# Optimization experiments

Hardware: AMD Instinct MI355X
Metric: run time of the kernel (lower is better)

## Reference

```python
import jax, jax.numpy as jnp
import numpy as np

N_NODES = 100000
N_EDGES = 1600000
D_IN = 128
D_HID = 128
N_CLASSES = 40


def _glorot(key, fan_in, fan_out):
    lim = np.sqrt(6.0 / (fan_in + fan_out)).astype(np.float32)
    return jax.random.uniform(key, (fan_in, fan_out), jnp.float32, -lim, lim)


def setup_inputs() -> dict:
    key = jax.random.key(0)
    ks = jax.random.split(key, 10)
    x = jax.random.normal(ks[0], (N_NODES, D_IN), jnp.float32)
    edge_index = jax.random.randint(ks[1], (2, N_EDGES), 0, N_NODES, jnp.int64)
    return {
        "x": x,
        "edge_index": edge_index,
        # layer 1: lin_l (neighbor, with bias), lin_r (root, no bias)
        "W1l": _glorot(ks[2], D_IN, D_HID),
        "b1": jnp.zeros((D_HID,), jnp.float32),
        "W1r": _glorot(ks[3], D_IN, D_HID),
        # layer 2
        "W2l": _glorot(ks[4], D_HID, D_HID),
        "b2": jnp.zeros((D_HID,), jnp.float32),
        "W2r": _glorot(ks[5], D_HID, D_HID),
        # layer 3
        "W3l": _glorot(ks[6], D_HID, N_CLASSES),
        "b3": jnp.zeros((N_CLASSES,), jnp.float32),
        "W3r": _glorot(ks[7], D_HID, N_CLASSES),
    }


def _sage_conv(x, src, dst, deg_inv, Wl, bl, Wr):
    # mean aggregation of source-node features onto destination nodes
    msgs = x[src]                                            # [E, d] gather
    agg = jax.ops.segment_sum(msgs, dst, num_segments=N_NODES)  # [N, d]
    agg = agg * deg_inv[:, None]                             # mean
    return agg @ Wl + bl + x @ Wr


def reference(x, edge_index, W1l, b1, W1r, W2l, b2, W2r, W3l, b3, W3r):
    src, dst = edge_index[0], edge_index[1]
    deg = jax.ops.segment_sum(jnp.ones((N_EDGES,), x.dtype), dst,
                              num_segments=N_NODES)
    deg_inv = 1.0 / jnp.maximum(deg, 1.0)
    h = _sage_conv(x, src, dst, deg_inv, W1l, b1, W1r)
    h = jax.nn.relu(h)  # dropout is identity in eval mode
    h = _sage_conv(h, src, dst, deg_inv, W2l, b2, W2r)
    h = jax.nn.relu(h)
    h = _sage_conv(h, src, dst, deg_inv, W3l, b3, W3r)
    return jax.nn.log_softmax(h, axis=1)
```

## Files before the change

kernel.cpp:

```cpp
#include <hip/hip_runtime.h>
#include <math.h>

#define D 128
#define NCLS 40
#define NBLK_P1 256

typedef unsigned int u32;
typedef __attribute__((ext_vector_type(8))) short short8;
typedef __attribute__((ext_vector_type(4))) float f32x4;

__device__ inline float bflo(u32 u){ return __uint_as_float(u << 16); }
__device__ inline float bfhi(u32 u){ return __uint_as_float(u & 0xffff0000u); }
__device__ inline u32 pack2bf(float a, float b){
  u32 ua = __float_as_uint(a), ub = __float_as_uint(b);
  ua += 0x7fffu + ((ua >> 16) & 1u);
  ub += 0x7fffu + ((ub >> 16) & 1u);
  return (ua >> 16) | (ub & 0xffff0000u);
}
__device__ inline unsigned short pack1bf(float a){
  u32 ua = __float_as_uint(a);
  ua += 0x7fffu + ((ua >> 16) & 1u);
  return (unsigned short)(ua >> 16);
}

__global__ __launch_bounds__(256) void prep_k(
    const float4* __restrict__ x4, uint2* __restrict__ xb, int n4,
    const float* __restrict__ W1l, const float* __restrict__ W1r, u32* __restrict__ Wt1,
    const float* __restrict__ W2l, const float* __restrict__ W2r, u32* __restrict__ Wt2,
    const float* __restrict__ W3l, const float* __restrict__ W3r,
    u32* __restrict__ Wt3b, float* __restrict__ bias3b, const float* __restrict__ b3,
    const int* __restrict__ dst, int* __restrict__ gcnt, int E, int nbuk, int nbX)
{
  __shared__ int cnt[1024];
  const int b = blockIdx.x;
  const int tid = threadIdx.x;
  if (b < nbX){
    int i = b * 256 + tid;
    if (i < n4){
      float4 v = x4[i];
      xb[i] = make_uint2(pack2bf(v.x, v.y), pack2bf(v.z, v.w));
    }
  } else if (b < nbX + 128){
    const bool first = (b < nbX + 64);
    const float* Wl = first ? W1l : W2l;
    const float* Wr = first ? W1r : W2r;
    u32* Wt = first ? Wt1 : Wt2;
    int i = ((b - nbX) & 63) * 256 + tid;
    int nn = i >> 7, kp = i & 127;
    int k = kp * 2;
    float a, c;
    if (k < 128){ a = Wl[(size_t)k * 128 + nn]; c = Wl[(size_t)(k + 1) * 128 + nn]; }
    else        { a = Wr[(size_t)(k - 128) * 128 + nn]; c = Wr[(size_t)(k - 127) * 128 + nn]; }
    Wt[(size_t)nn * 128 + kp] = pack2bf(a, c);
  } else if (b < nbX + 160){
    int i = (b - nbX - 128) * 256 + tid;
    if (i < 128 * 64){
      int nn = i >> 6, kp = i & 63;
      int k = kp * 2;
      float a = 0.f, c = 0.f;
      if (nn < NCLS){
        a = W3l[(size_t)k * NCLS + nn]; c = W3l[(size_t)(k + 1) * NCLS + nn];
      } else if (nn >= 64 && nn < 64 + NCLS){
        int cc = nn - 64;
        a = W3r[(size_t)k * NCLS + cc]; c = W3r[(size_t)(k + 1) * NCLS + cc];
      }
      Wt3b[(size_t)nn * 64 + kp] = pack2bf(a, c);
    }
    if (b == nbX + 128 && tid < 128)
      bias3b[tid] = (tid >= 64 && tid < 64 + NCLS) ? b3[tid - 64] : 0.f;
  } else {
    const int hb = b - nbX - 160;
    for (int i = tid; i < nbuk; i += 256) cnt[i] = 0;
    __syncthreads();
    const int per = (E + NBLK_P1 - 1) / NBLK_P1;
    const int e0 = hb * per;
    const int e1 = min(e0 + per, E);
    for (int i = e0 + tid; i < e1; i += 256)
      atomicAdd(&cnt[dst[i] >> 7], 1);
    __syncthreads();
    for (int i = tid; i < nbuk; i += 256)
      gcnt[(size_t)hb * nbuk + i] = cnt[i];
  }
}

__global__ __launch_bounds__(256) void colscan_k(
    const int* __restrict__ gcnt, int* __restrict__ goff,
    int* __restrict__ btot, int nbuk)
{
  __shared__ int sm[256];
  const int j = blockIdx.x;
  const int i = threadIdx.x;
  int v = gcnt[(size_t)i * nbuk + j];
  sm[i] = v;
  __syncthreads();
  int acc = v;
  for (int off = 1; off < 256; off <<= 1){
    int t = (i >= off) ? sm[i - off] : 0;
    __syncthreads();
    acc += t; sm[i] = acc;
    __syncthreads();
  }
  goff[(size_t)i * nbuk + j] = acc - v;
  if (i == 255) btot[j] = acc;
}

__global__ __launch_bounds__(1024) void scan_k(
    const int* __restrict__ btot, int* __restrict__ bbase, int nbuk)
{
  __shared__ int sm[1024];
  const int j = threadIdx.x;
  int v = (j < nbuk) ? btot[j] : 0;
  sm[j] = v;
  __syncthreads();
  int acc = v;
  for (int off = 1; off < 1024; off <<= 1){
    int t = (j >= off) ? sm[j - off] : 0;
    __syncthreads();
    acc += t; sm[j] = acc;
    __syncthreads();
  }
  if (j < nbuk){
    bbase[j] = acc - v;
    if (j == nbuk - 1) bbase[nbuk] = acc;
  }
}

__global__ __launch_bounds__(256) void part_fill_k(
    const int* __restrict__ src, const int* __restrict__ dst,
    const int* __restrict__ goff, const int* __restrict__ bbase,
    u32* __restrict__ staging, int E, int nbuk)
{
  __shared__ int boff[1024];
  __shared__ int cur[1024];
  const int tid = threadIdx.x;
  for (int i = tid; i < nbuk; i += 256){
    boff[i] = goff[(size_t)blockIdx.x * nbuk + i] + bbase[i];
    cur[i] = 0;
  }
  __syncthreads();
  const int per = (E + NBLK_P1 - 1) / NBLK_P1;
  const int e0 = blockIdx.x * per;
  const int e1 = min(e0 + per, E);
  for (int i = e0 + tid; i < e1; i += 256){
    int d = dst[i];
    int s = src[i];
    int b = d >> 7;
    int p = atomicAdd(&cur[b], 1);
    staging[boff[b] + p] = ((u32)s << 7) | (u32)(d & 127);
  }
}

__global__ __launch_bounds__(256) void bucket_csr_k(
    const u32* __restrict__ staging, const int* __restrict__ bbase,
    int* __restrict__ csr_off, float* __restrict__ deg_inv,
    int* __restrict__ csr_src, int N)
{
  __shared__ int ldeg[128];
  __shared__ int sm[128];
  __shared__ int lbase[128];
  __shared__ int lpos[128];
  const int b = blockIdx.x;
  const int node0 = b << 7;
  const int tid = threadIdx.x;
  if (tid < 128) ldeg[tid] = 0;
  __syncthreads();
  const int lo = bbase[b], hi = bbase[b + 1];
  for (int i = lo + tid; i < hi; i += 256)
    atomicAdd(&ldeg[staging[i] & 127u], 1);
  __syncthreads();
  if (tid < 128) sm[tid] = ldeg[tid];
  __syncthreads();
  for (int off = 1; off < 128; off <<= 1){
    int t = (tid >= off && tid < 128) ? sm[tid - off] : 0;
    __syncthreads();
    if (tid < 128) sm[tid] += t;
    __syncthreads();
  }
  if (tid < 128){
    const int excl = sm[tid] - ldeg[tid];
    lbase[tid] = lo + excl;
    lpos[tid] = 0;
    const int node = node0 + tid;
    if (node < N){
      csr_off[node] = lo + excl;
      deg_inv[node] = 1.0f / fmaxf((float)ldeg[tid], 1.0f);
    } else if (node == N){
      csr_off[N] = lo + excl;
    }
  }
  if (tid == 0 && b == (int)gridDim.x - 1) csr_off[N] = hi;
  __syncthreads();
  for (int i = lo + tid; i < hi; i += 256){
    u32 v = staging[i];
    int dloc = (int)(v & 127u);
    int p = atomicAdd(&lpos[dloc], 1);
    csr_src[lbase[dloc] + p] = (int)(v >> 7);
  }
}

__device__ inline void add8(float* acc, uint4 v){
  acc[0] += bflo(v.x); acc[1] += bfhi(v.x);
  acc[2] += bflo(v.y); acc[3] += bfhi(v.y);
  acc[4] += bflo(v.z); acc[5] += bfhi(v.z);
  acc[6] += bflo(v.w); acc[7] += bfhi(v.w);
}

__global__ __launch_bounds__(256) void aggregate_k(
    const u32* __restrict__ feat, const int* __restrict__ coff,
    const int* __restrict__ csr_src, const float* __restrict__ deg_inv,
    u32* __restrict__ agg, int n)
{
  const int g = threadIdx.x >> 4;
  const int lane = threadIdx.x & 15;
  const int node = blockIdx.x * 16 + g;
  if (node >= n) return;
  const int lo = coff[node], hi = coff[node + 1];
  const uint4* __restrict__ f4 = (const uint4*)feat;
  float acc[8] = {0.f,0.f,0.f,0.f,0.f,0.f,0.f,0.f};
  int e = lo;
  for (; e + 7 < hi; e += 8){
    int s0 = csr_src[e],     s1 = csr_src[e + 1];
    int s2 = csr_src[e + 2], s3 = csr_src[e + 3];
    int s4 = csr_src[e + 4], s5 = csr_src[e + 5];
    int s6 = csr_src[e + 6], s7 = csr_src[e + 7];
    uint4 v0 = f4[(size_t)s0 * 16 + lane];
    uint4 v1 = f4[(size_t)s1 * 16 + lane];
    uint4 v2 = f4[(size_t)s2 * 16 + lane];
    uint4 v3 = f4[(size_t)s3 * 16 + lane];
    uint4 v4 = f4[(size_t)s4 * 16 + lane];
    uint4 v5 = f4[(size_t)s5 * 16 + lane];
    uint4 v6 = f4[(size_t)s6 * 16 + lane];
    uint4 v7 = f4[(size_t)s7 * 16 + lane];
    add8(acc, v0); add8(acc, v1); add8(acc, v2); add8(acc, v3);
    add8(acc, v4); add8(acc, v5); add8(acc, v6); add8(acc, v7);
  }
  for (; e + 3 < hi; e += 4){
    int s0 = csr_src[e],     s1 = csr_src[e + 1];
    int s2 = csr_src[e + 2], s3 = csr_src[e + 3];
    uint4 v0 = f4[(size_t)s0 * 16 + lane];
    uint4 v1 = f4[(size_t)s1 * 16 + lane];
    uint4 v2 = f4[(size_t)s2 * 16 + lane];
    uint4 v3 = f4[(size_t)s3 * 16 + lane];
    add8(acc, v0); add8(acc, v1); add8(acc, v2); add8(acc, v3);
  }
  for (; e < hi; ++e){
    uint4 v0 = f4[(size_t)csr_src[e] * 16 + lane];
    add8(acc, v0);
  }
  const float di = deg_inv[node];
  uint4 o;
  o.x = pack2bf(acc[0] * di, acc[1] * di);
  o.y = pack2bf(acc[2] * di, acc[3] * di);
  o.z = pack2bf(acc[4] * di, acc[5] * di);
  o.w = pack2bf(acc[6] * di, acc[7] * di);
  ((uint4*)agg)[(size_t)node * 16 + lane] = o;
}

__global__ __launch_bounds__(256) void gemm_mfma_k(
    const u32* __restrict__ A1, const u32* __restrict__ A2,
    const u32* __restrict__ Wt, const float* __restrict__ bias,
    u32* __restrict__ out, int n)
{
  __shared__ u32 smem[8704];
  u32* As_u = smem;
  u32* Bs_u = smem + 2560;
  const int tid = threadIdx.x;
  const int row0 = blockIdx.x * 128;
  const int l = tid & 63, w = tid >> 6;
  const int lm = l & 15, lq = l >> 4;

  f32x4 acc[2][8];
  #pragma unroll
  for (int mi = 0; mi < 2; mi++)
    #pragma unroll
    for (int ni = 0; ni < 8; ni++) acc[mi][ni] = (f32x4){0.f, 0.f, 0.f, 0.f};

  for (int kt = 0; kt < 8; ++kt){
    const u32* Ap = (kt < 4) ? A1 : A2;
    const int ko = (kt & 3) * 16;
    #pragma unroll
    for (int i = 0; i < 2; i++){
      int chunk = tid + 256 * i;
      int row = chunk >> 2, q = chunk & 3;
      uint4 av = make_uint4(0, 0, 0, 0);
      int gr = row0 + row;
      if (gr < n) av = *(const uint4*)(Ap + (size_t)gr * 64 + ko + q * 4);
      *(uint4*)&As_u[row * 20 + q * 4] = av;
      uint4 bv = *(const uint4*)(Wt + (size_t)row * 128 + kt * 16 + q * 4);
      *(uint4*)&Bs_u[row * 20 + q * 4] = bv;
    }
    __syncthreads();
    short8 af0 = *(const short8*)&As_u[(w * 32 + lm) * 20 + lq * 4];
    short8 af1 = *(const short8*)&As_u[(w * 32 + 16 + lm) * 20 + lq * 4];
    #pragma unroll
    for (int ni = 0; ni < 8; ni++){
      short8 bf = *(const short8*)&Bs_u[(ni * 16 + lm) * 20 + lq * 4];
      acc[0][ni] = __builtin_amdgcn_mfma_f32_16x16x32_bf16(af0, bf, acc[0][ni], 0, 0, 0);
      acc[1][ni] = __builtin_amdgcn_mfma_f32_16x16x32_bf16(af1, bf, acc[1][ni], 0, 0, 0);
    }
    __syncthreads();
  }

  float bb[8];
  #pragma unroll
  for (int ni = 0; ni < 8; ni++) bb[ni] = bias[ni * 16 + lm];
  unsigned short* es = (unsigned short*)smem + w * (32 * 136);
  #pragma unroll
  for (int mi = 0; mi < 2; mi++)
    #pragma unroll
    for (int r = 0; r < 4; r++){
      const int Lr = mi * 16 + lq * 4 + r;
      #pragma unroll
      for (int ni = 0; ni < 8; ni++){
        float v = fmaxf(acc[mi][ni][r] + bb[ni], 0.f);
        es[Lr * 136 + ni * 16 + lm] = pack1bf(v);
      }
    }
  __syncthreads();
  uint4* outv = (uint4*)out;
  const int cl = l & 15;
  const int rsub = l >> 4;
  #pragma unroll
  for (int p = 0; p < 8; p++){
    const int Lr = p * 4 + rsub;
    const int row = row0 + w * 32 + Lr;
    uint4 t = *(const uint4*)&es[Lr * 136 + cl * 8];
    if (row < n) outv[(size_t)row * 16 + cl] = t;
  }
}

__global__ __launch_bounds__(256) void gemm23_mfma_k(
    const u32* __restrict__ A1, const u32* __restrict__ A2,
    const u32* __restrict__ Wt2, const float* __restrict__ b2,
    const u32* __restrict__ Wt3b, const float* __restrict__ bias3b,
    u32* __restrict__ yz, int n)
{
  __shared__ u32 Bs[128 * 20];
  __shared__ u32 big[8704];
  u32* As = big;
  unsigned short* esH = (unsigned short*)big;
  const int tid = threadIdx.x;
  const int row0 = blockIdx.x * 128;
  const int l = tid & 63, w = tid >> 6;
  const int lm = l & 15, lq = l >> 4;

  f32x4 acc[2][8];
  #pragma unroll
  for (int mi = 0; mi < 2; mi++)
    #pragma unroll
    for (int ni = 0; ni < 8; ni++) acc[mi][ni] = (f32x4){0.f, 0.f, 0.f, 0.f};

  for (int kt = 0; kt < 8; ++kt){
    const u32* Ap = (kt < 4) ? A1 : A2;
    const int ko = (kt & 3) * 16;
    #pragma unroll
    for (int i = 0; i < 2; i++){
      int chunk = tid + 256 * i;
      int row = chunk >> 2, q = chunk & 3;
      uint4 av = make_uint4(0, 0, 0, 0);
      int gr = row0 + row;
      if (gr < n) av = *(const uint4*)(Ap + (size_t)gr * 64 + ko + q * 4);
      *(uint4*)&As[row * 20 + q * 4] = av;
      uint4 bv = *(const uint4*)(Wt2 + (size_t)row * 128 + kt * 16 + q * 4);
      *(uint4*)&Bs[row * 20 + q * 4] = bv;
    }
    __syncthreads();
    short8 af0 = *(const short8*)&As[(w * 32 + lm) * 20 + lq * 4];
    short8 af1 = *(const short8*)&As[(w * 32 + 16 + lm) * 20 + lq * 4];
    #pragma unroll
    for (int ni = 0; ni < 8; ni++){
      short8 bf = *(const short8*)&Bs[(ni * 16 + lm) * 20 + lq * 4];
      acc[0][ni] = __builtin_amdgcn_mfma_f32_16x16x32_bf16(af0, bf, acc[0][ni], 0, 0, 0);
      acc[1][ni] = __builtin_amdgcn_mfma_f32_16x16x32_bf16(af1, bf, acc[1][ni], 0, 0, 0);
    }
    __syncthreads();
  }

  {
    float bb[8];
    #pragma unroll
    for (int ni = 0; ni < 8; ni++) bb[ni] = b2[ni * 16 + lm];
    #pragma unroll
    for (int mi = 0; mi < 2; mi++)
      #pragma unroll
      for (int r = 0; r < 4; r++){
        const int grow = w * 32 + mi * 16 + lq * 4 + r;
        #pragma unroll
        for (int ni = 0; ni < 8; ni++){
          float v = fmaxf(acc[mi][ni][r] + bb[ni], 0.f);
          esH[grow * 136 + ni * 16 + lm] = pack1bf(v);
        }
      }
  }
  __syncthreads();

  f32x4 acc2[2][8];
  #pragma unroll
  for (int mi = 0; mi < 2; mi++)
    #pragma unroll
    for (int ni = 0; ni < 8; ni++) acc2[mi][ni] = (f32x4){0.f, 0.f, 0.f, 0.f};

  for (int kt = 0; kt < 4; ++kt){
    #pragma unroll
    for (int i = 0; i < 2; i++){
      int c2 = tid + 256 * i;
      int brow = c2 >> 2, q = c2 & 3;
      uint4 bv = *(const uint4*)(Wt3b + (size_t)brow * 64 + kt * 16 + q * 4);
      *(uint4*)&Bs[brow * 20 + q * 4] = bv;
    }
    __syncthreads();
    short8 a0 = *(const short8*)&esH[(w * 32 + lm) * 136 + kt * 32 + lq * 8];
    short8 a1 = *(const short8*)&esH[(w * 32 + 16 + lm) * 136 + kt * 32 + lq * 8];
    #pragma unroll
    for (int ni = 0; ni < 8; ni++){
      short8 bf = *(const short8*)&Bs[(ni * 16 + lm) * 20 + lq * 4];
      acc2[0][ni] = __builtin_amdgcn_mfma_f32_16x16x32_bf16(a0, bf, acc2[0][ni], 0, 0, 0);
      acc2[1][ni] = __builtin_amdgcn_mfma_f32_16x16x32_bf16(a1, bf, acc2[1][ni], 0, 0, 0);
    }
    __syncthreads();
  }

  {
    float bb3[8];
    #pragma unroll
    for (int ni = 0; ni < 8; ni++) bb3[ni] = bias3b[ni * 16 + lm];
    #pragma unroll
    for (int mi = 0; mi < 2; mi++)
      #pragma unroll
      for (int r = 0; r < 4; r++){
        const int grow = w * 32 + mi * 16 + lq * 4 + r;
        #pragma unroll
        for (int ni = 0; ni < 8; ni++){
          float v = acc2[mi][ni][r] + bb3[ni];
          esH[grow * 136 + ni * 16 + lm] = pack1bf(v);
        }
      }
  }
  __syncthreads();
  uint4* outv = (uint4*)yz;
  const int cl = l & 15;
  const int rsub = l >> 4;
  #pragma unroll
  for (int p = 0; p < 8; p++){
    const int Lr = p * 4 + rsub;
    const int row = row0 + w * 32 + Lr;
    uint4 t = *(const uint4*)&esH[(w * 32 + Lr) * 136 + cl * 8];
    if (row < n) outv[(size_t)row * 16 + cl] = t;
  }
}

__global__ __launch_bounds__(256) void agg_softmax_k(
    const u32* __restrict__ yz, const int* __restrict__ coff,
    const int* __restrict__ csr_src, const float* __restrict__ deg_inv,
    float* __restrict__ out, int n)
{
  const int g = threadIdx.x >> 3;
  const int lane = threadIdx.x & 7;
  const int node = blockIdx.x * 32 + g;
  if (node >= n) return;
  const int lo = coff[node], hi = coff[node + 1];
  const uint4* __restrict__ f4 = (const uint4*)yz;
  float acc[8] = {0.f,0.f,0.f,0.f,0.f,0.f,0.f,0.f};
  int e = lo;
  for (; e + 7 < hi; e += 8){
    int s0 = csr_src[e],     s1 = csr_src[e + 1];
    int s2 = csr_src[e + 2], s3 = csr_src[e + 3];
    int s4 = csr_src[e + 4], s5 = csr_src[e + 5];
    int s6 = csr_src[e + 6], s7 = csr_src[e + 7];
    uint4 v0 = f4[(size_t)s0 * 16 + lane];
    uint4 v1 = f4[(size_t)s1 * 16 + lane];
    uint4 v2 = f4[(size_t)s2 * 16 + lane];
    uint4 v3 = f4[(size_t)s3 * 16 + lane];
    uint4 v4 = f4[(size_t)s4 * 16 + lane];
    uint4 v5 = f4[(size_t)s5 * 16 + lane];
    uint4 v6 = f4[(size_t)s6 * 16 + lane];
    uint4 v7 = f4[(size_t)s7 * 16 + lane];
    add8(acc, v0); add8(acc, v1); add8(acc, v2); add8(acc, v3);
    add8(acc, v4); add8(acc, v5); add8(acc, v6); add8(acc, v7);
  }
  for (; e + 3 < hi; e += 4){
    int s0 = csr_src[e],     s1 = csr_src[e + 1];
    int s2 = csr_src[e + 2], s3 = csr_src[e + 3];
    uint4 v0 = f4[(size_t)s0 * 16 + lane];
    uint4 v1 = f4[(size_t)s1 * 16 + lane];
    uint4 v2 = f4[(size_t)s2 * 16 + lane];
    uint4 v3 = f4[(size_t)s3 * 16 + lane];
    add8(acc, v0); add8(acc, v1); add8(acc, v2); add8(acc, v3);
  }
  for (; e < hi; ++e){
    uint4 v0 = f4[(size_t)csr_src[e] * 16 + lane];
    add8(acc, v0);
  }
  const float di = deg_inv[node];
  uint4 zv = f4[(size_t)node * 16 + 8 + lane];
  float v[8];
  v[0] = acc[0] * di + bflo(zv.x); v[1] = acc[1] * di + bfhi(zv.x);
  v[2] = acc[2] * di + bflo(zv.y); v[3] = acc[3] * di + bfhi(zv.y);
  v[4] = acc[4] * di + bflo(zv.z); v[5] = acc[5] * di + bfhi(zv.z);
  v[6] = acc[6] * di + bflo(zv.w); v[7] = acc[7] * di + bfhi(zv.w);
  const bool valid = (lane < 5);
  float m = -INFINITY;
  if (valid){
    #pragma unroll
    for (int j = 0; j < 8; j++) m = fmaxf(m, v[j]);
  }
  #pragma unroll
  for (int off = 1; off < 8; off <<= 1) m = fmaxf(m, __shfl_xor(m, off, 64));
  float s = 0.f;
  if (valid){
    #pragma unroll
    for (int j = 0; j < 8; j++) s += __expf(v[j] - m);
  }
  #pragma unroll
  for (int off = 1; off < 8; off <<= 1) s += __shfl_xor(s, off, 64);
  const float ls = m + logf(s);
  if (valid){
    float* op = out + (size_t)node * NCLS + lane * 8;
    *(float4*)op     = make_float4(v[0]-ls, v[1]-ls, v[2]-ls, v[3]-ls);
    *(float4*)(op+4) = make_float4(v[4]-ls, v[5]-ls, v[6]-ls, v[7]-ls);
  }
}


extern "C" void kernel_launch(void* const* d_in, const int* in_sizes, int n_in,
                              void* d_out, int out_size, void* d_ws, size_t ws_size,
                              hipStream_t stream) {
  const float* x   = (const float*)d_in[0];
  const int*   ei  = (const int*)d_in[1];
  const float* W1l = (const float*)d_in[2];
  const float* b1  = (const float*)d_in[3];
  const float* W1r = (const float*)d_in[4];
  const float* W2l = (const float*)d_in[5];
  const float* b2  = (const float*)d_in[6];
  const float* W2r = (const float*)d_in[7];
  const float* W3l = (const float*)d_in[8];
  const float* b3  = (const float*)d_in[9];
  const float* W3r = (const float*)d_in[10];

  const int N = in_sizes[0] / D;
  const int E = in_sizes[1] / 2;
  const int* src = ei;
  const int* dst = ei + E;
  const int nbuk = (N + 127) >> 7;

  char* ws = (char*)d_ws;
  auto alloc = [&](size_t bytes) -> void* {
    void* p = (void*)ws;
    ws += (bytes + 255) & ~(size_t)255;
    return p;
  };
  int*   csr_off  = (int*)  alloc((size_t)(N + 1) * 4);
  float* deg_inv  = (float*)alloc((size_t)N * 4);
  int*   csr_src  = (int*)  alloc((size_t)E * 4);
  u32*   staging  = (u32*)  alloc((size_t)E * 4);
  int*   gcnt     = (int*)  alloc((size_t)NBLK_P1 * nbuk * 4);
  int*   goff     = (int*)  alloc((size_t)NBLK_P1 * nbuk * 4);
  int*   bbase    = (int*)  alloc((size_t)(nbuk + 1) * 4);
  int*   btot     = (int*)  alloc((size_t)(nbuk + 1) * 4);
  u32*   xb       = (u32*)  alloc((size_t)N * D * 2);
  u32*   agg      = (u32*)  alloc((size_t)N * D * 2);
  u32*   hbuf     = (u32*)  alloc((size_t)N * D * 2);
  u32*   yz       = (u32*)  alloc((size_t)N * D * 2);
  u32*   Wt1      = (u32*)  alloc((size_t)128 * 128 * 4);
  u32*   Wt2      = (u32*)  alloc((size_t)128 * 128 * 4);
  u32*   Wt3b     = (u32*)  alloc((size_t)128 * 64 * 4);
  float* bias3b   = (float*)alloc((size_t)128 * 4);

  const int n4 = N * D / 4;
  const int nbX = (n4 + 255) / 256;
  prep_k<<<nbX + 160 + NBLK_P1, 256, 0, stream>>>(
      (const float4*)x, (uint2*)xb, n4,
      W1l, W1r, Wt1, W2l, W2r, Wt2,
      W3l, W3r, Wt3b, bias3b, b3,
      dst, gcnt, E, nbuk, nbX);

  colscan_k<<<nbuk, 256, 0, stream>>>(gcnt, goff, btot, nbuk);
  scan_k<<<1, 1024, 0, stream>>>(btot, bbase, nbuk);
  part_fill_k<<<NBLK_P1, 256, 0, stream>>>(src, dst, goff, bbase, staging, E, nbuk);
  bucket_csr_k<<<nbuk, 256, 0, stream>>>(staging, bbase, csr_off, deg_inv, csr_src, N);

  const int gblocks = (N + 127) / 128;
  const int ablocks = (N + 15) / 16;
  aggregate_k<<<ablocks, 256, 0, stream>>>(xb, csr_off, csr_src, deg_inv, agg, N);
  gemm_mfma_k<<<gblocks, 256, 0, stream>>>(agg, xb, Wt1, b1, hbuf, N);
  aggregate_k<<<ablocks, 256, 0, stream>>>(hbuf, csr_off, csr_src, deg_inv, agg, N);
  gemm23_mfma_k<<<gblocks, 256, 0, stream>>>(agg, hbuf, Wt2, b2, Wt3b, bias3b, yz, N);
  agg_softmax_k<<<(N + 31) / 32, 256, 0, stream>>>(yz, csr_off, csr_src, deg_inv,
                                                   (float*)d_out, N);
}
```

Before: 367.9 us.

## Fuse CSR build into cooperative kernel and overlap root GEMM with aggregation

Merges the four CSR-construction kernels (column scan, bucket scan, partition fill, bucket CSR) into one cooperative kernel separated by grid syncs, which removes several launch gaps. It also splits each layer's GEMM so the root term x@Wr runs in the same launch as the neighbor aggregation. Those two block types run side by side, and the fp32 root result is written to a scratch buffer that the following GEMM adds back. The cost is an extra fp32 N×128 write and read per layer, plus grid-sync overhead in the cooperative kernel.

Result: slower. 743.5 us (+102.1%).

```diff
diff --git a/kernel.cpp b/kernel.cpp
--- a/kernel.cpp
+++ b/kernel.cpp
@@ -1,5 +1,8 @@
 #include <hip/hip_runtime.h>
+#include <hip/hip_cooperative_groups.h>
 #include <math.h>
+
+namespace cg = cooperative_groups;
 
 #define D 128
 #define NCLS 40
@@ -83,118 +86,124 @@
   }
 }
 
-__global__ __launch_bounds__(256) void colscan_k(
+__global__ __launch_bounds__(256) void csr_build_k(
     const int* __restrict__ gcnt, int* __restrict__ goff,
-    int* __restrict__ btot, int nbuk)
+    int* __restrict__ btot, int* __restrict__ bbase,
+    const int* __restrict__ src, const int* __restrict__ dst,
+    u32* __restrict__ staging, int* __restrict__ csr_off,
+    float* __restrict__ deg_inv, int* __restrict__ csr_src,
+    int E, int N, int nbuk)
 {
-  __shared__ int sm[256];
-  const int j = blockIdx.x;
-  const int i = threadIdx.x;
-  int v = gcnt[(size_t)i * nbuk + j];
-  sm[i] = v;
-  __syncthreads();
-  int acc = v;
-  for (int off = 1; off < 256; off <<= 1){
-    int t = (i >= off) ? sm[i - off] : 0;
-    __syncthreads();
-    acc += t; sm[i] = acc;
-    __syncthreads();
-  }
-  goff[(size_t)i * nbuk + j] = acc - v;
-  if (i == 255) btot[j] = acc;
-}
-
-__global__ __launch_bounds__(1024) void scan_k(
-    const int* __restrict__ btot, int* __restrict__ bbase, int nbuk)
-{
-  __shared__ int sm[1024];
-  const int j = threadIdx.x;
-  int v = (j < nbuk) ? btot[j] : 0;
-  sm[j] = v;
-  __syncthreads();
-  int acc = v;
-  for (int off = 1; off < 1024; off <<= 1){
-    int t = (j >= off) ? sm[j - off] : 0;
-    __syncthreads();
-    acc += t; sm[j] = acc;
-    __syncthreads();
-  }
-  if (j < nbuk){
-    bbase[j] = acc - v;
-    if (j == nbuk - 1) bbase[nbuk] = acc;
-  }
-}
-
-__global__ __launch_bounds__(256) void part_fill_k(
-    const int* __restrict__ src, const int* __restrict__ dst,
-    const int* __restrict__ goff, const int* __restrict__ bbase,
-    u32* __restrict__ staging, int E, int nbuk)
-{
-  __shared__ int boff[1024];
-  __shared__ int cur[1024];
+  cg::grid_group grid = cg::this_grid();
+  __shared__ int sm[2048];
+  const int b = blockIdx.x;
   const int tid = threadIdx.x;
-  for (int i = tid; i < nbuk; i += 256){
-    boff[i] = goff[(size_t)blockIdx.x * nbuk + i] + bbase[i];
-    cur[i] = 0;
-  }
-  __syncthreads();
-  const int per = (E + NBLK_P1 - 1) / NBLK_P1;
-  const int e0 = blockIdx.x * per;
-  const int e1 = min(e0 + per, E);
-  for (int i = e0 + tid; i < e1; i += 256){
-    int d = dst[i];
-    int s = src[i];
-    int b = d >> 7;
-    int p = atomicAdd(&cur[b], 1);
-    staging[boff[b] + p] = ((u32)s << 7) | (u32)(d & 127);
-  }
-}
-
-__global__ __launch_bounds__(256) void bucket_csr_k(
-    const u32* __restrict__ staging, const int* __restrict__ bbase,
-    int* __restrict__ csr_off, float* __restrict__ deg_inv,
-    int* __restrict__ csr_src, int N)
-{
-  __shared__ int ldeg[128];
-  __shared__ int sm[128];
-  __shared__ int lbase[128];
-  __shared__ int lpos[128];
-  const int b = blockIdx.x;
-  const int node0 = b << 7;
-  const int tid = threadIdx.x;
-  if (tid < 128) ldeg[tid] = 0;
-  __syncthreads();
-  const int lo = bbase[b], hi = bbase[b + 1];
-  for (int i = lo + tid; i < hi; i += 256)
-    atomicAdd(&ldeg[staging[i] & 127u], 1);
-  __syncthreads();
-  if (tid < 128) sm[tid] = ldeg[tid];
-  __syncthreads();
-  for (int off = 1; off < 128; off <<= 1){
-    int t = (tid >= off && tid < 128) ? sm[tid - off] : 0;
-    __syncthreads();
-    if (tid < 128) sm[tid] += t;
-    __syncthreads();
-  }
-  if (tid < 128){
-    const int excl = sm[tid] - ldeg[tid];
-    lbase[tid] = lo + excl;
-    lpos[tid] = 0;
-    const int node = node0 + tid;
-    if (node < N){
-      csr_off[node] = lo + excl;
-      deg_inv[node] = 1.0f / fmaxf((float)ldeg[tid], 1.0f);
-    } else if (node == N){
-      csr_off[N] = lo + excl;
-    }
-  }
-  if (tid == 0 && b == (int)gridDim.x - 1) csr_off[N] = hi;
-  __syncthreads();
-  for (int i = lo + tid; i < hi; i += 256){
-    u32 v = staging[i];
-    int dloc = (int)(v & 127u);
-    int p = atomicAdd(&lpos[dloc], 1);
-    csr_src[lbase[dloc] + p] = (int)(v >> 7);
+
+  if (b < nbuk){
+    int v = gcnt[(size_t)tid * nbuk + b];
+    sm[tid] = v;
+    __syncthreads();
+    int acc = v;
+    for (int off = 1; off < 256; off <<= 1){
+      int t = (tid >= off) ? sm[tid - off] : 0;
+      __syncthreads();
+      acc += t; sm[tid] = acc;
+      __syncthreads();
+    }
+    goff[(size_t)tid * nbuk + b] = acc - v;
+    if (tid == 255) btot[b] = acc;
+  }
+  grid.sync();
+
+  if (b == 0){
+    int v[4]; int s = 0;
+    #pragma unroll
+    for (int j = 0; j < 4; j++){
+      int idx = tid * 4 + j;
+      v[j] = (idx < nbuk) ? btot[idx] : 0;
+      s += v[j];
+    }
+    sm[tid] = s;
+    __syncthreads();
+    int acc = s;
+    for (int off = 1; off < 256; off <<= 1){
+      int t = (tid >= off) ? sm[tid - off] : 0;
+      __syncthreads();
+      acc += t; sm[tid] = acc;
+      __syncthreads();
+    }
+    int run = acc - s;
+    #pragma unroll
+    for (int j = 0; j < 4; j++){
+      int idx = tid * 4 + j;
+      if (idx < nbuk) bbase[idx] = run;
+      run += v[j];
+    }
+    if (tid == 255) bbase[nbuk] = run;
+  }
+  grid.sync();
+
+  if (b < NBLK_P1){
+    int* boff = sm;
+    int* cur  = sm + 1024;
+    for (int i = tid; i < nbuk; i += 256){
+      boff[i] = goff[(size_t)b * nbuk + i] + bbase[i];
+      cur[i] = 0;
+    }
+    __syncthreads();
+    const int per = (E + NBLK_P1 - 1) / NBLK_P1;
+    const int e0 = b * per;
+    const int e1 = min(e0 + per, E);
+    for (int i = e0 + tid; i < e1; i += 256){
+      int d = dst[i];
+      int s2 = src[i];
+      int bk = d >> 7;
+      int p = atomicAdd(&cur[bk], 1);
+      staging[boff[bk] + p] = ((u32)s2 << 7) | (u32)(d & 127);
+    }
+  }
+  grid.sync();
+
+  if (b < nbuk){
+    int* ldeg  = sm;
+    int* sm2   = sm + 128;
+    int* lbase = sm + 256;
+    int* lpos  = sm + 384;
+    const int node0 = b << 7;
+    if (tid < 128) ldeg[tid] = 0;
+    __syncthreads();
+    const int lo = bbase[b], hi = bbase[b + 1];
+    for (int i = lo + tid; i < hi; i += 256)
+      atomicAdd(&ldeg[staging[i] & 127u], 1);
+    __syncthreads();
+    if (tid < 128) sm2[tid] = ldeg[tid];
+    __syncthreads();
+    for (int off = 1; off < 128; off <<= 1){
+      int t = (tid >= off && tid < 128) ? sm2[tid - off] : 0;
+      __syncthreads();
+      if (tid < 128) sm2[tid] += t;
+      __syncthreads();
+    }
+    if (tid < 128){
+      const int excl = sm2[tid] - ldeg[tid];
+      lbase[tid] = lo + excl;
+      lpos[tid] = 0;
+      const int node = node0 + tid;
+      if (node < N){
+        csr_off[node] = lo + excl;
+        deg_inv[node] = 1.0f / fmaxf((float)ldeg[tid], 1.0f);
+      } else if (node == N){
+        csr_off[N] = lo + excl;
+      }
+    }
+    if (tid == 0 && b == nbuk - 1) csr_off[N] = hi;
+    __syncthreads();
+    for (int i = lo + tid; i < hi; i += 256){
+      u32 v = staging[i];
+      int dloc = (int)(v & 127u);
+      int p = atomicAdd(&lpos[dloc], 1);
+      csr_src[lbase[dloc] + p] = (int)(v >> 7);
+    }
   }
 }
 
@@ -205,14 +214,14 @@
   acc[6] += bflo(v.w); acc[7] += bfhi(v.w);
 }
 
-__global__ __launch_bounds__(256) void aggregate_k(
+__device__ __forceinline__ void agg_body(
     const u32* __restrict__ feat, const int* __restrict__ coff,
     const int* __restrict__ csr_src, const float* __restrict__ deg_inv,
-    u32* __restrict__ agg, int n)
+    u32* __restrict__ agg, int n, int blk)
 {
   const int g = threadIdx.x >> 4;
   const int lane = threadIdx.x & 15;
-  const int node = blockIdx.x * 16 + g;
+  const int node = blk * 16 + g;
   if (node >= n) return;
   const int lo = coff[node], hi = coff[node + 1];
   const uint4* __restrict__ f4 = (const uint4*)feat;
@@ -256,14 +265,19 @@
   ((uint4*)agg)[(size_t)node * 16 + lane] = o;
 }
 
-__global__ __launch_bounds__(256) void gemm_mfma_k(
-    const u32* __restrict__ A1, const u32* __restrict__ A2,
-    const u32* __restrict__ Wt, const float* __restrict__ bias,
-    u32* __restrict__ out, int n)
+__global__ __launch_bounds__(256) void agg_xr_k(
+    const u32* __restrict__ feat, const int* __restrict__ coff,
+    const int* __restrict__ csr_src, const float* __restrict__ deg_inv,
+    u32* __restrict__ agg, const u32* __restrict__ Wt, float* __restrict__ xr,
+    int n, int gblocks)
 {
-  __shared__ u32 smem[8704];
-  u32* As_u = smem;
-  u32* Bs_u = smem + 2560;
+  __shared__ u32 smem[5120];
+  if ((int)blockIdx.x >= gblocks){
+    agg_body(feat, coff, csr_src, deg_inv, agg, n, blockIdx.x - gblocks);
+    return;
+  }
+  u32* As = smem;
+  u32* Bs = smem + 2560;
   const int tid = threadIdx.x;
   const int row0 = blockIdx.x * 128;
   const int l = tid & 63, w = tid >> 6;
@@ -275,31 +289,82 @@
     #pragma unroll
     for (int ni = 0; ni < 8; ni++) acc[mi][ni] = (f32x4){0.f, 0.f, 0.f, 0.f};
 
-  for (int kt = 0; kt < 8; ++kt){
-    const u32* Ap = (kt < 4) ? A1 : A2;
-    const int ko = (kt & 3) * 16;
+  for (int kt = 0; kt < 4; ++kt){
     #pragma unroll
     for (int i = 0; i < 2; i++){
       int chunk = tid + 256 * i;
       int row = chunk >> 2, q = chunk & 3;
       uint4 av = make_uint4(0, 0, 0, 0);
       int gr = row0 + row;
-      if (gr < n) av = *(const uint4*)(Ap + (size_t)gr * 64 + ko + q * 4);
-      *(uint4*)&As_u[row * 20 + q * 4] = av;
-      uint4 bv = *(const uint4*)(Wt + (size_t)row * 128 + kt * 16 + q * 4);
-      *(uint4*)&Bs_u[row * 20 + q * 4] = bv;
-    }
-    __syncthreads();
-    short8 af0 = *(const short8*)&As_u[(w * 32 + lm) * 20 + lq * 4];
-    short8 af1 = *(const short8*)&As_u[(w * 32 + 16 + lm) * 20 + lq * 4];
+      if (gr < n) av = *(const uint4*)(feat + (size_t)gr * 64 + kt * 16 + q * 4);
+      *(uint4*)&As[row * 20 + q * 4] = av;
+      uint4 bv = *(const uint4*)(Wt + (size_t)row * 128 + 64 + kt * 16 + q * 4);
+      *(uint4*)&Bs[row * 20 + q * 4] = bv;
+    }
+    __syncthreads();
+    short8 af0 = *(const short8*)&As[(w * 32 + lm) * 20 + lq * 4];
+    short8 af1 = *(const short8*)&As[(w * 32 + 16 + lm) * 20 + lq * 4];
     #pragma unroll
     for (int ni = 0; ni < 8; ni++){
-      short8 bf = *(const short8*)&Bs_u[(ni * 16 + lm) * 20 + lq * 4];
+      short8 bf = *(const short8*)&Bs[(ni * 16 + lm) * 20 + lq * 4];
       acc[0][ni] = __builtin_amdgcn_mfma_f32_16x16x32_bf16(af0, bf, acc[0][ni], 0, 0, 0);
       acc[1][ni] = __builtin_amdgcn_mfma_f32_16x16x32_bf16(af1, bf, acc[1][ni], 0, 0, 0);
     }
     __syncthreads();
   }
+  #pragma unroll
+  for (int mi = 0; mi < 2; mi++)
+    #pragma unroll
+    for (int r = 0; r < 4; r++){
+      const int row = row0 + w * 32 + mi * 16 + lq * 4 + r;
+      #pragma unroll
+      for (int ni = 0; ni < 8; ni++)
+        xr[(size_t)row * 128 + ni * 16 + lm] = acc[mi][ni][r];
+    }
+}
+
+__global__ __launch_bounds__(256) void gemm_l_k(
+    const u32* __restrict__ A, const u32* __restrict__ Wt,
+    const float* __restrict__ xr, const float* __restrict__ bias,
+    u32* __restrict__ out, int n)
+{
+  __shared__ u32 smem[8704];
+  u32* As = smem;
+  u32* Bs = smem + 2560;
+  const int tid = threadIdx.x;
+  const int row0 = blockIdx.x * 128;
+  const int l = tid & 63, w = tid >> 6;
+  const int lm = l & 15, lq = l >> 4;
+
+  f32x4 acc[2][8];
+  #pragma unroll
+  for (int mi = 0; mi < 2; mi++)
+    #pragma unroll
+    for (int ni = 0; ni < 8; ni++) acc[mi][ni] = (f32x4){0.f, 0.f, 0.f, 0.f};
+
+  for (int kt = 0; kt < 4; ++kt){
+    #pragma unroll
+    for (int i = 0; i < 2; i++){
+      int chunk = tid + 256 * i;
+      int row = chunk >> 2, q = chunk & 3;
+      uint4 av = make_uint4(0, 0, 0, 0);
+      int gr = row0 + row;
+      if (gr < n) av = *(const uint4*)(A + (size_t)gr * 64 + kt * 16 + q * 4);
+      *(uint4*)&As[row * 20 + q * 4] = av;
+      uint4 bv = *(const uint4*)(Wt + (size_t)row * 128 + kt * 16 + q * 4);
+      *(uint4*)&Bs[row * 20 + q * 4] = bv;
+    }
+    __syncthreads();
+    short8 af0 = *(const short8*)&As[(w * 32 + lm) * 20 + lq * 4];
+    short8 af1 = *(const short8*)&As[(w * 32 + 16 + lm) * 20 + lq * 4];
+    #pragma unroll
+    for (int ni = 0; ni < 8; ni++){
+      short8 bf = *(const short8*)&Bs[(ni * 16 + lm) * 20 + lq * 4];
+      acc[0][ni] = __builtin_amdgcn_mfma_f32_16x16x32_bf16(af0, bf, acc[0][ni], 0, 0, 0);
+      acc[1][ni] = __builtin_amdgcn_mfma_f32_16x16x32_bf16(af1, bf, acc[1][ni], 0, 0, 0);
+    }
+    __syncthreads();
+  }
 
   float bb[8];
   #pragma unroll
@@ -310,9 +375,10 @@
     #pragma unroll
     for (int r = 0; r < 4; r++){
       const int Lr = mi * 16 + lq * 4 + r;
+      const int row = row0 + w * 32 + Lr;
       #pragma unroll
       for (int ni = 0; ni < 8; ni++){
-        float v = fmaxf(acc[mi][ni][r] + bb[ni], 0.f);
+        float v = fmaxf(acc[mi][ni][r] + xr[(size_t)row * 128 + ni * 16 + lm] + bb[ni], 0.f);
         es[Lr * 136 + ni * 16 + lm] = pack1bf(v);
       }
     }
@@ -330,8 +396,8 @@
 }
 
 __global__ __launch_bounds__(256) void gemm23_mfma_k(
-    const u32* __restrict__ A1, const u32* __restrict__ A2,
-    const u32* __restrict__ Wt2, const float* __restrict__ b2,
+    const u32* __restrict__ A, const u32* __restrict__ Wt2,
+    const float* __restrict__ xr, const float* __restrict__ b2,
     const u32* __restrict__ Wt3b, const float* __restrict__ bias3b,
     u32* __restrict__ yz, int n)
 {
@@ -350,16 +416,14 @@
     #pragma unroll
     for (int ni = 0; ni < 8; ni++) acc[mi][ni] = (f32x4){0.f, 0.f, 0.f, 0.f};
 
-  for (int kt = 0; kt < 8; ++kt){
-    const u32* Ap = (kt < 4) ? A1 : A2;
-    const int ko = (kt & 3) * 16;
+  for (int kt = 0; kt < 4; ++kt){
     #pragma unroll
     for (int i = 0; i < 2; i++){
       int chunk = tid + 256 * i;
       int row = chunk >> 2, q = chunk & 3;
       uint4 av = make_uint4(0, 0, 0, 0);
       int gr = row0 + row;
-      if (gr < n) av = *(const uint4*)(Ap + (size_t)gr * 64 + ko + q * 4);
+      if (gr < n) av = *(const uint4*)(A + (size_t)gr * 64 + kt * 16 + q * 4);
       *(uint4*)&As[row * 20 + q * 4] = av;
       uint4 bv = *(const uint4*)(Wt2 + (size_t)row * 128 + kt * 16 + q * 4);
       *(uint4*)&Bs[row * 20 + q * 4] = bv;
@@ -385,9 +449,10 @@
       #pragma unroll
       for (int r = 0; r < 4; r++){
         const int grow = w * 32 + mi * 16 + lq * 4 + r;
+        const int row = row0 + grow;
         #pragma unroll
         for (int ni = 0; ni < 8; ni++){
-          float v = fmaxf(acc[mi][ni][r] + bb[ni], 0.f);
+          float v = fmaxf(acc[mi][ni][r] + xr[(size_t)row * 128 + ni * 16 + lm] + bb[ni], 0.f);
           esH[grow * 136 + ni * 16 + lm] = pack1bf(v);
         }
       }
@@ -549,6 +614,8 @@
     ws += (bytes + 255) & ~(size_t)255;
     return p;
   };
+  const int gblocks = (N + 127) / 128;
+  const int ablocks = (N + 15) / 16;
   int*   csr_off  = (int*)  alloc((size_t)(N + 1) * 4);
   float* deg_inv  = (float*)alloc((size_t)N * 4);
   int*   csr_src  = (int*)  alloc((size_t)E * 4);
@@ -561,6 +628,7 @@
   u32*   agg      = (u32*)  alloc((size_t)N * D * 2);
   u32*   hbuf     = (u32*)  alloc((size_t)N * D * 2);
   u32*   yz       = (u32*)  alloc((size_t)N * D * 2);
+  float* xr       = (float*)alloc((size_t)gblocks * 128 * 128 * 4);
   u32*   Wt1      = (u32*)  alloc((size_t)128 * 128 * 4);
   u32*   Wt2      = (u32*)  alloc((size_t)128 * 128 * 4);
   u32*   Wt3b     = (u32*)  alloc((size_t)128 * 64 * 4);
@@ -574,17 +642,22 @@
       W3l, W3r, Wt3b, bias3b, b3,
       dst, gcnt, E, nbuk, nbX);
 
-  colscan_k<<<nbuk, 256, 0, stream>>>(gcnt, goff, btot, nbuk);
-  scan_k<<<1, 1024, 0, stream>>>(btot, bbase, nbuk);
-  part_fill_k<<<NBLK_P1, 256, 0, stream>>>(src, dst, goff, bbase, staging, E, nbuk);
-  bucket_csr_k<<<nbuk, 256, 0, stream>>>(staging, bbase, csr_off, deg_inv, csr_src, N);
-
-  const int gblocks = (N + 127) / 128;
-  const int ablocks = (N + 15) / 16;
-  aggregate_k<<<ablocks, 256, 0, stream>>>(xb, csr_off, csr_src, deg_inv, agg, N);
-  gemm_mfma_k<<<gblocks, 256, 0, stream>>>(agg, xb, Wt1, b1, hbuf, N);
-  aggregate_k<<<ablocks, 256, 0, stream>>>(hbuf, csr_off, csr_src, deg_inv, agg, N);
-  gemm23_mfma_k<<<gblocks, 256, 0, stream>>>(agg, hbuf, Wt2, b2, Wt3b, bias3b, yz, N);
+  {
+    int Ev = E, Nv = N, nbv = nbuk;
+    void* args[] = { (void*)&gcnt, (void*)&goff, (void*)&btot, (void*)&bbase,
+                     (void*)&src, (void*)&dst, (void*)&staging, (void*)&csr_off,
+                     (void*)&deg_inv, (void*)&csr_src, &Ev, &Nv, &nbv };
+    const int cgrid = (nbuk > NBLK_P1) ? nbuk : NBLK_P1;
+    hipLaunchCooperativeKernel((const void*)csr_build_k, dim3(cgrid), dim3(256),
+                               args, 0, stream);
+  }
+
+  agg_xr_k<<<gblocks + ablocks, 256, 0, stream>>>(xb, csr_off, csr_src, deg_inv,
+                                                  agg, Wt1, xr, N, gblocks);
+  gemm_l_k<<<gblocks, 256, 0, stream>>>(agg, Wt1, xr, b1, hbuf, N);
+  agg_xr_k<<<gblocks + ablocks, 256, 0, stream>>>(hbuf, csr_off, csr_src, deg_inv,
+                                                  agg, Wt2, xr, N, gblocks);
+  gemm23_mfma_k<<<gblocks, 256, 0, stream>>>(agg, Wt2, xr, b2, Wt3b, bias3b, yz, N);
   agg_softmax_k<<<(N + 31) / 32, 256, 0, stream>>>(yz, csr_off, csr_src, deg_inv,
                                                    (float*)d_out, N);
 }
```

## Fuse CSR build kernels into one persistent kernel with grid barriers

Applied to the files above, without the earlier changes.

Merges the column scan, bucket scan, partition fill and per-bucket CSR kernels into a single 256-block kernel that separates phases with a software grid barrier using global atomics. The barrier counters are reset inside the preceding prep kernel. This removes three kernel launches and the idle gaps between them. In exchange, bucket-level work now runs on only 256 blocks in a loop, the single-block scan sits between two barriers, and correctness depends on all 256 blocks being co-resident.

New measurement: 510.7 us. 38.8% more time.

```diff
diff --git a/kernel.cpp b/kernel.cpp
--- a/kernel.cpp
+++ b/kernel.cpp
@@ -29,7 +29,8 @@
     const float* __restrict__ W2l, const float* __restrict__ W2r, u32* __restrict__ Wt2,
     const float* __restrict__ W3l, const float* __restrict__ W3r,
     u32* __restrict__ Wt3b, float* __restrict__ bias3b, const float* __restrict__ b3,
-    const int* __restrict__ dst, int* __restrict__ gcnt, int E, int nbuk, int nbX)
+    const int* __restrict__ dst, int* __restrict__ gcnt, int* __restrict__ syncw,
+    int E, int nbuk, int nbX)
 {
   __shared__ int cnt[1024];
   const int b = blockIdx.x;
@@ -70,6 +71,7 @@
       bias3b[tid] = (tid >= 64 && tid < 64 + NCLS) ? b3[tid - 64] : 0.f;
   } else {
     const int hb = b - nbX - 160;
+    if (hb == 0 && tid == 0){ syncw[0] = 0; syncw[1] = 0; }
     for (int i = tid; i < nbuk; i += 256) cnt[i] = 0;
     __syncthreads();
     const int per = (E + NBLK_P1 - 1) / NBLK_P1;
@@ -83,118 +85,144 @@
   }
 }
 
-__global__ __launch_bounds__(256) void colscan_k(
+__device__ __forceinline__ void gbarrier(int* cnt, int* gen, int nblk){
+  __threadfence();
+  __syncthreads();
+  if (threadIdx.x == 0){
+    int g = atomicAdd(gen, 0);
+    if (atomicAdd(cnt, 1) == nblk - 1){
+      atomicExch(cnt, 0);
+      __threadfence();
+      atomicAdd(gen, 1);
+    } else {
+      while (atomicAdd(gen, 0) == g){ __builtin_amdgcn_s_sleep(8); }
+    }
+    __threadfence();
+  }
+  __syncthreads();
+}
+
+__global__ __launch_bounds__(256) void csr1_k(
     const int* __restrict__ gcnt, int* __restrict__ goff,
-    int* __restrict__ btot, int nbuk)
+    int* __restrict__ btot, int* __restrict__ bbase,
+    const int* __restrict__ src, const int* __restrict__ dst,
+    u32* __restrict__ staging, int* __restrict__ csr_off,
+    float* __restrict__ deg_inv, int* __restrict__ csr_src,
+    int* __restrict__ syncw, int E, int N, int nbuk)
 {
-  __shared__ int sm[256];
-  const int j = blockIdx.x;
-  const int i = threadIdx.x;
-  int v = gcnt[(size_t)i * nbuk + j];
-  sm[i] = v;
-  __syncthreads();
-  int acc = v;
-  for (int off = 1; off < 256; off <<= 1){
-    int t = (i >= off) ? sm[i - off] : 0;
-    __syncthreads();
-    acc += t; sm[i] = acc;
-    __syncthreads();
-  }
-  goff[(size_t)i * nbuk + j] = acc - v;
-  if (i == 255) btot[j] = acc;
-}
-
-__global__ __launch_bounds__(1024) void scan_k(
-    const int* __restrict__ btot, int* __restrict__ bbase, int nbuk)
-{
-  __shared__ int sm[1024];
-  const int j = threadIdx.x;
-  int v = (j < nbuk) ? btot[j] : 0;
-  sm[j] = v;
-  __syncthreads();
-  int acc = v;
-  for (int off = 1; off < 1024; off <<= 1){
-    int t = (j >= off) ? sm[j - off] : 0;
-    __syncthreads();
-    acc += t; sm[j] = acc;
-    __syncthreads();
-  }
-  if (j < nbuk){
-    bbase[j] = acc - v;
-    if (j == nbuk - 1) bbase[nbuk] = acc;
-  }
-}
-
-__global__ __launch_bounds__(256) void part_fill_k(
-    const int* __restrict__ src, const int* __restrict__ dst,
-    const int* __restrict__ goff, const int* __restrict__ bbase,
-    u32* __restrict__ staging, int E, int nbuk)
-{
-  __shared__ int boff[1024];
-  __shared__ int cur[1024];
+  __shared__ int sm[2048];
   const int tid = threadIdx.x;
-  for (int i = tid; i < nbuk; i += 256){
-    boff[i] = goff[(size_t)blockIdx.x * nbuk + i] + bbase[i];
-    cur[i] = 0;
-  }
-  __syncthreads();
-  const int per = (E + NBLK_P1 - 1) / NBLK_P1;
-  const int e0 = blockIdx.x * per;
-  const int e1 = min(e0 + per, E);
-  for (int i = e0 + tid; i < e1; i += 256){
-    int d = dst[i];
-    int s = src[i];
-    int b = d >> 7;
-    int p = atomicAdd(&cur[b], 1);
-    staging[boff[b] + p] = ((u32)s << 7) | (u32)(d & 127);
-  }
-}
-
-__global__ __launch_bounds__(256) void bucket_csr_k(
-    const u32* __restrict__ staging, const int* __restrict__ bbase,
-    int* __restrict__ csr_off, float* __restrict__ deg_inv,
-    int* __restrict__ csr_src, int N)
-{
-  __shared__ int ldeg[128];
-  __shared__ int sm[128];
-  __shared__ int lbase[128];
-  __shared__ int lpos[128];
   const int b = blockIdx.x;
-  const int node0 = b << 7;
-  const int tid = threadIdx.x;
-  if (tid < 128) ldeg[tid] = 0;
-  __syncthreads();
-  const int lo = bbase[b], hi = bbase[b + 1];
-  for (int i = lo + tid; i < hi; i += 256)
-    atomicAdd(&ldeg[staging[i] & 127u], 1);
-  __syncthreads();
-  if (tid < 128) sm[tid] = ldeg[tid];
-  __syncthreads();
-  for (int off = 1; off < 128; off <<= 1){
-    int t = (tid >= off && tid < 128) ? sm[tid - off] : 0;
-    __syncthreads();
-    if (tid < 128) sm[tid] += t;
-    __syncthreads();
-  }
-  if (tid < 128){
-    const int excl = sm[tid] - ldeg[tid];
-    lbase[tid] = lo + excl;
-    lpos[tid] = 0;
-    const int node = node0 + tid;
-    if (node < N){
-      csr_off[node] = lo + excl;
-      deg_inv[node] = 1.0f / fmaxf((float)ldeg[tid], 1.0f);
-    } else if (node == N){
-      csr_off[N] = lo + excl;
-    }
-  }
-  if (tid == 0 && b == (int)gridDim.x - 1) csr_off[N] = hi;
-  __syncthreads();
-  for (int i = lo + tid; i < hi; i += 256){
-    u32 v = staging[i];
-    int dloc = (int)(v & 127u);
-    int p = atomicAdd(&lpos[dloc], 1);
-    csr_src[lbase[dloc] + p] = (int)(v >> 7);
+  int* cnt = syncw;
+  int* gen = syncw + 1;
+
+  for (int jb = b; jb < nbuk; jb += NBLK_P1){
+    int v = gcnt[(size_t)tid * nbuk + jb];
+    sm[tid] = v;
+    __syncthreads();
+    int acc = v;
+    for (int off = 1; off < 256; off <<= 1){
+      int t = (tid >= off) ? sm[tid - off] : 0;
+      __syncthreads();
+      acc += t; sm[tid] = acc;
+      __syncthreads();
+    }
+    goff[(size_t)tid * nbuk + jb] = acc - v;
+    if (tid == 255) btot[jb] = acc;
+    __syncthreads();
+  }
+  gbarrier(cnt, gen, NBLK_P1);
+
+  if (b == 0){
+    int v[4]; int s = 0;
+    #pragma unroll
+    for (int j = 0; j < 4; j++){
+      int idx = tid * 4 + j;
+      v[j] = (idx < nbuk) ? btot[idx] : 0;
+      s += v[j];
+    }
+    sm[tid] = s;
+    __syncthreads();
+    int acc = s;
+    for (int off = 1; off < 256; off <<= 1){
+      int t = (tid >= off) ? sm[tid - off] : 0;
+      __syncthreads();
+      acc += t; sm[tid] = acc;
+      __syncthreads();
+    }
+    int run = acc - s;
+    #pragma unroll
+    for (int j = 0; j < 4; j++){
+      int idx = tid * 4 + j;
+      if (idx < nbuk) bbase[idx] = run;
+      run += v[j];
+    }
+    if (tid == 255) bbase[nbuk] = run;
+  }
+  gbarrier(cnt, gen, NBLK_P1);
+
+  {
+    int* boff = sm;
+    int* cur  = sm + 1024;
+    for (int i = tid; i < nbuk; i += 256){
+      boff[i] = goff[(size_t)b * nbuk + i] + bbase[i];
+      cur[i] = 0;
+    }
+    __syncthreads();
+    const int per = (E + NBLK_P1 - 1) / NBLK_P1;
+    const int e0 = b * per;
+    const int e1 = min(e0 + per, E);
+    for (int i = e0 + tid; i < e1; i += 256){
+      int d = dst[i];
+      int s2 = src[i];
+      int bk = d >> 7;
+      int p = atomicAdd(&cur[bk], 1);
+      staging[boff[bk] + p] = ((u32)s2 << 7) | (u32)(d & 127);
+    }
+  }
+  gbarrier(cnt, gen, NBLK_P1);
+
+  for (int jb = b; jb < nbuk; jb += NBLK_P1){
+    int* ldeg  = sm;
+    int* sm2   = sm + 128;
+    int* lbase = sm + 256;
+    int* lpos  = sm + 384;
+    const int node0 = jb << 7;
+    if (tid < 128) ldeg[tid] = 0;
+    __syncthreads();
+    const int lo = bbase[jb], hi = bbase[jb + 1];
+    for (int i = lo + tid; i < hi; i += 256)
+      atomicAdd(&ldeg[staging[i] & 127u], 1);
+    __syncthreads();
+    if (tid < 128) sm2[tid] = ldeg[tid];
+    __syncthreads();
+    for (int off = 1; off < 128; off <<= 1){
+      int t = (tid >= off && tid < 128) ? sm2[tid - off] : 0;
+      __syncthreads();
+      if (tid < 128) sm2[tid] += t;
+      __syncthreads();
+    }
+    if (tid < 128){
+      const int excl = sm2[tid] - ldeg[tid];
+      lbase[tid] = lo + excl;
+      lpos[tid] = 0;
+      const int node = node0 + tid;
+      if (node < N){
+        csr_off[node] = lo + excl;
+        deg_inv[node] = 1.0f / fmaxf((float)ldeg[tid], 1.0f);
+      } else if (node == N){
+        csr_off[N] = lo + excl;
+      }
+    }
+    if (tid == 0 && jb == nbuk - 1) csr_off[N] = hi;
+    __syncthreads();
+    for (int i = lo + tid; i < hi; i += 256){
+      u32 v = staging[i];
+      int dloc = (int)(v & 127u);
+      int p = atomicAdd(&lpos[dloc], 1);
+      csr_src[lbase[dloc] + p] = (int)(v >> 7);
+    }
+    __syncthreads();
   }
 }
 
@@ -557,6 +585,7 @@
   int*   goff     = (int*)  alloc((size_t)NBLK_P1 * nbuk * 4);
   int*   bbase    = (int*)  alloc((size_t)(nbuk + 1) * 4);
   int*   btot     = (int*)  alloc((size_t)(nbuk + 1) * 4);
+  int*   syncw    = (int*)  alloc(256);
   u32*   xb       = (u32*)  alloc((size_t)N * D * 2);
   u32*   agg      = (u32*)  alloc((size_t)N * D * 2);
   u32*   hbuf     = (u32*)  alloc((size_t)N * D * 2);
@@ -572,12 +601,10 @@
       (const float4*)x, (uint2*)xb, n4,
       W1l, W1r, Wt1, W2l, W2r, Wt2,
       W3l, W3r, Wt3b, bias3b, b3,
-      dst, gcnt, E, nbuk, nbX);
-
-  colscan_k<<<nbuk, 256, 0, stream>>>(gcnt, goff, btot, nbuk);
-  scan_k<<<1, 1024, 0, stream>>>(btot, bbase, nbuk);
-  part_fill_k<<<NBLK_P1, 256, 0, stream>>>(src, dst, goff, bbase, staging, E, nbuk);
-  bucket_csr_k<<<nbuk, 256, 0, stream>>>(staging, bbase, csr_off, deg_inv, csr_src, N);
+      dst, gcnt, syncw, E, nbuk, nbX);
+
+  csr1_k<<<NBLK_P1, 256, 0, stream>>>(gcnt, goff, btot, bbase, src, dst, staging,
+                                      csr_off, deg_inv, csr_src, syncw, E, N, nbuk);
 
   const int gblocks = (N + 127) / 128;
   const int ablocks = (N + 15) / 16;
```
